# Performance work log

Measured on AMD Instinct MI355X. Metric: run time of the kernel, lower is better.

## Reference

```python
import jax, jax.numpy as jnp
import numpy as np

N = 10000      # nodes (= num_spatial_nodes)
E = 320000     # edges
IN = 4         # in_channels
HID = 256      # hidden_channels
H1, C1 = 4, 64 # conv1: heads, per-head out (hidden//heads)
EDIM = 1       # edge_feature_size
EPS = 1e-5


def _layernorm(x, g, b):
    mu = jnp.mean(x, axis=-1, keepdims=True)
    var = jnp.mean(jnp.square(x - mu), axis=-1, keepdims=True)
    return (x - mu) / jnp.sqrt(var + EPS) * g + b


def _gatv2(x, src, dst, ea, Wl, bl, Wr, br, We, att, bias, H, C, n):
    # PyG GATv2Conv: lin_l on source, lin_r on target, lin_edge on edge_attr
    xl = (x @ Wl + bl).reshape(n, H, C)
    xr = (x @ Wr + br).reshape(n, H, C)
    ee = (ea @ We).reshape(-1, H, C)
    m = jax.nn.leaky_relu(xl[src] + xr[dst] + ee, 0.2)   # [E', H, C]
    logit = jnp.einsum('ehc,hc->eh', m, att)             # [E', H]
    # segment softmax over incoming edges of each dst node
    mx = jax.ops.segment_max(logit, dst, num_segments=n)
    ex = jnp.exp(logit - mx[dst])
    den = jax.ops.segment_sum(ex, dst, num_segments=n)
    alpha = ex / den[dst]
    out = jax.ops.segment_sum(xl[src] * alpha[:, :, None], dst, num_segments=n)
    return out.reshape(n, H * C) + bias


def setup_inputs() -> dict:
    key = jax.random.key(0)
    ks = jax.random.split(key, 32)
    gl = lambda k, shape, fan: (jax.random.normal(k, shape, jnp.float32) / np.sqrt(fan)).astype(jnp.float32)
    inp = {}
    inp['x'] = jax.random.normal(ks[0], (N, IN), jnp.float32)
    inp['edge_index'] = jax.random.randint(ks[1], (2, E), 0, N, jnp.int32)
    inp['edge_attr'] = jax.random.normal(ks[2], (E, EDIM), jnp.float32)
    # conv1 (heads=4, out=64, concat -> 256)
    inp['Wl1'] = gl(ks[3], (IN, HID), IN);  inp['bl1'] = jnp.zeros((HID,), jnp.float32)
    inp['Wr1'] = gl(ks[4], (IN, HID), IN);  inp['br1'] = jnp.zeros((HID,), jnp.float32)
    inp['We1'] = gl(ks[5], (EDIM, HID), EDIM)
    inp['att1'] = gl(ks[6], (H1, C1), C1)
    inp['bias1'] = jnp.zeros((HID,), jnp.float32)
    inp['g1'] = jnp.ones((HID,), jnp.float32); inp['be1'] = jnp.zeros((HID,), jnp.float32)
    # conv2 (heads=1, out=256)
    inp['Wl2'] = gl(ks[7], (HID, HID), HID); inp['bl2'] = jnp.zeros((HID,), jnp.float32)
    inp['Wr2'] = gl(ks[8], (HID, HID), HID); inp['br2'] = jnp.zeros((HID,), jnp.float32)
    inp['We2'] = gl(ks[9], (EDIM, HID), EDIM)
    inp['att2'] = gl(ks[10], (1, HID), HID)
    inp['bias2'] = jnp.zeros((HID,), jnp.float32)
    inp['g2'] = jnp.ones((HID,), jnp.float32); inp['be2'] = jnp.zeros((HID,), jnp.float32)
    # policy head
    inp['Wp1'] = gl(ks[11], (HID, HID // 2), HID); inp['bp1'] = jnp.zeros((HID // 2,), jnp.float32)
    inp['Wp2'] = gl(ks[12], (HID // 2, IN), HID // 2); inp['bp2'] = jnp.zeros((IN,), jnp.float32)
    return inp


def reference(x, edge_index, edge_attr,
              Wl1, bl1, Wr1, br1, We1, att1, bias1, g1, be1,
              Wl2, bl2, Wr2, br2, We2, att2, bias2, g2, be2,
              Wp1, bp1, Wp2, bp2):
    src, dst = edge_index[0], edge_index[1]
    # add_self_loops with fill_value='mean': loop edge_attr = mean of incoming edge_attr
    deg = jax.ops.segment_sum(jnp.ones((E,), jnp.float32), dst, num_segments=N)
    loop_attr = jax.ops.segment_sum(edge_attr, dst, num_segments=N) / jnp.maximum(deg, 1.0)[:, None]
    ar = jnp.arange(N, dtype=src.dtype)
    src_a = jnp.concatenate([src, ar]); dst_a = jnp.concatenate([dst, ar])
    ea_a = jnp.concatenate([edge_attr, loop_attr], axis=0)
    h = _gatv2(x, src_a, dst_a, ea_a, Wl1, bl1, Wr1, br1, We1, att1, bias1, H1, C1, N)
    h = jax.nn.relu(_layernorm(h, g1, be1))
    h = _gatv2(h, src_a, dst_a, ea_a, Wl2, bl2, Wr2, br2, We2, att2, bias2, 1, HID, N)
    h = jax.nn.relu(_layernorm(h, g2, be2))
    logits = jax.nn.relu(h @ Wp1 + bp1) @ Wp2 + bp2   # [N, IN]
    return jax.nn.softmax(logits.reshape(1, -1), axis=1)
```

## Files before the change

kernel.cpp:

```cpp
#include <hip/hip_runtime.h>
#include <math.h>

#define N_NODES 10000
#define N_EDGES 320000
#define N_AUG   (N_EDGES + N_NODES)
#define CPK_CAP 330752
#define HID     256

typedef short short8 __attribute__((ext_vector_type(8)));
typedef float floatx16 __attribute__((ext_vector_type(16)));

static __device__ __forceinline__ unsigned bf16rne(float f) {
  unsigned u = __float_as_uint(f);
  return (u + 0x7FFFu + ((u >> 16) & 1u)) >> 16;
}

__global__ void __launch_bounds__(256) k_front(
    const int* __restrict__ dst, const float* __restrict__ ea,
    unsigned long long* __restrict__ pdeg, int* __restrict__ rank,
    const float* __restrict__ W1, const float* __restrict__ W2,
    const float* __restrict__ Wp1,
    unsigned short* __restrict__ Wt, unsigned short* __restrict__ Wp1t) {
  __shared__ float tile[32][33];
  int bi = blockIdx.x;
// ... 49 lines not shown
  for (int i = 0; i < 40; i++) {
    int n = base + i;
    if (n < N_NODES) s += (int)(pdeg[n] >> 32) + 1;
  }
  int v = s;
  #pragma unroll
  for (int d = 1; d < 64; d <<= 1) {
    int u = __shfl_up(v, d);
    if ((t & 63) >= d) v += u;
  }
  if ((t & 63) == 63) wsum[t >> 6] = v;
  __syncthreads();
  int wb = 0;
  for (int i = 0; i < (t >> 6); i++) wb += wsum[i];
  int run = wb + v - s;
  for (int i = 0; i < 40; i++) {
    int n = base + i;
    if (n < N_NODES) {
      offs[n] = run;
      unsigned long long pv = pdeg[n];
      int d = (int)(pv >> 32);
      run += d + 1;
      int lower = (int)(pv & 0xFFFFFFFFull);
      float asum = (float)(lower - d * 2097152) * (1.f / 262144.f);
      lattr[n] = asum / (float)max(d, 1);
    }
  }
  if (t == 255) offs[N_NODES] = wb + v;
}

__global__ void k_scatter(const int* __restrict__ src, const int* __restrict__ dst,
                          const float* __restrict__ ea, const float* __restrict__ lattr,
                          const int* __restrict__ offs, const int* __restrict__ rank,
                          int2* __restrict__ cpk) {
  int e = blockIdx.x * blockDim.x + threadIdx.x;
  if (e >= N_AUG) {
    if (e < CPK_CAP) cpk[e] = make_int2(0, 0);
    return;
  }
  int pos, s; float a;
  if (e < N_EDGES) {
    s = src[e];
    int d = dst[e];
    a = ea[e];
    pos = offs[d] + rank[e];
  } else {
    s = e - N_EDGES;
    a = lattr[s];
    pos = offs[s + 1] - 1;
  }
  cpk[pos] = make_int2(s, __float_as_int(a));
}

#define C1_EDGE(xs, av, l0, l1, l2, l3, p)                                              \
  {                                                                                     \
    l0 = fmaf(xs.x,wl0.x, fmaf(xs.y,wl1.x, fmaf(xs.z,wl2.x, fmaf(xs.w,wl3.x, blv.x)))); \
    l1 = fmaf(xs.x,wl0.y, fmaf(xs.y,wl1.y, fmaf(xs.z,wl2.y, fmaf(xs.w,wl3.y, blv.y)))); \
    l2 = fmaf(xs.x,wl0.z, fmaf(xs.y,wl1.z, fmaf(xs.z,wl2.z, fmaf(xs.w,wl3.z, blv.z)))); \
    l3 = fmaf(xs.x,wl0.w, fmaf(xs.y,wl1.w, fmaf(xs.z,wl2.w, fmaf(xs.w,wl3.w, blv.w)))); \
    float m0 = l0 + fmaf(av, we.x, r4.x); m0 = fmaxf(m0, 0.2f*m0);                      \
    float m1 = l1 + fmaf(av, we.y, r4.y); m1 = fmaxf(m1, 0.2f*m1);                      \
    float m2 = l2 + fmaf(av, we.z, r4.z); m2 = fmaxf(m2, 0.2f*m2);                      \
    float m3 = l3 + fmaf(av, we.w, r4.w); m3 = fmaxf(m3, 0.2f*m3);                      \
    p = m0*at.x + m1*at.y + m2*at.z + m3*at.w;                                          \
  }

#define C1_BODY8()                                                              \
  {                                                                             \
    float avA = __int_as_float(eA.y), avB = __int_as_float(eB.y);               \
    float avC = __int_as_float(eC.y), avD = __int_as_float(eD.y);               \
    float avE = __int_as_float(eE.y), avF = __int_as_float(eF.y);               \
    float avG = __int_as_float(eG.y), avH = __int_as_float(eH.y);               \
    float lA0,lA1,lA2,lA3,pA, lB0,lB1,lB2,lB3,pB;                               \
    float lC0,lC1,lC2,lC3,pC, lD0,lD1,lD2,lD3,pD;                               \
    float lE0,lE1,lE2,lE3,pE, lF0,lF1,lF2,lF3,pF;                               \
    float lG0,lG1,lG2,lG3,pG, lH0,lH1,lH2,lH3,pH;                               \
    C1_EDGE(xA, avA, lA0,lA1,lA2,lA3, pA);                                      \
    C1_EDGE(xB, avB, lB0,lB1,lB2,lB3, pB);                                      \
    C1_EDGE(xC, avC, lC0,lC1,lC2,lC3, pC);                                      \
    C1_EDGE(xD, avD, lD0,lD1,lD2,lD3, pD);                                      \
    C1_EDGE(xE, avE, lE0,lE1,lE2,lE3, pE);                                      \
    C1_EDGE(xF, avF, lF0,lF1,lF2,lF3, pF);                                      \
    C1_EDGE(xG, avG, lG0,lG1,lG2,lG3, pG);                                      \
    C1_EDGE(xH, avH, lH0,lH1,lH2,lH3, pH);                                      \
    float sAB = b1 ? pA : pB, kAB = b1 ? pB : pA;                               \
    float qAB = kAB + __shfl_xor(sAB, 1);                                       \
    float sCD = b1 ? pC : pD, kCD = b1 ? pD : pC;                               \
    float qCD = kCD + __shfl_xor(sCD, 1);                                       \
    float sEF = b1 ? pE : pF, kEF = b1 ? pF : pE;                               \
    float qEF = kEF + __shfl_xor(sEF, 1);                                       \
    float sGH = b1 ? pG : pH, kGH = b1 ? pH : pG;                               \
    float qGH = kGH + __shfl_xor(sGH, 1);                                       \
    float u0s = b2 ? qAB : qCD, u0k = b2 ? qCD : qAB;                           \
    float u0 = u0k + __shfl_xor(u0s, 2);                                        \
    float u1s = b2 ? qEF : qGH, u1k = b2 ? qGH : qEF;                           \
    float u1 = u1k + __shfl_xor(u1s, 2);                                        \
    float vvs = b4 ? u0 : u1, vvk = b4 ? u1 : u0;                               \
    float vv = vvk + __shfl_xor(vvs, 4);                                        \
    vv += __shfl_xor(vv, 8);                                                    \
    float exv = expf(vv);                                                       \
    float xAe = __shfl(exv, 0, 16), xBe = __shfl(exv, 1, 16);                   \
    float xCe = __shfl(exv, 2, 16), xDe = __shfl(exv, 3, 16);                   \
    float xEe = __shfl(exv, 4, 16), xFe = __shfl(exv, 5, 16);                   \
    float xGe = __shfl(exv, 6, 16), xHe = __shfl(exv, 7, 16);                   \
    D += ((xAe + xBe) + (xCe + xDe)) + ((xEe + xFe) + (xGe + xHe));             \
    a0 = fmaf(xDe, lD0, fmaf(xCe, lC0, fmaf(xBe, lB0, fmaf(xAe, lA0, a0))));    \
    a0 = fmaf(xHe, lH0, fmaf(xGe, lG0, fmaf(xFe, lF0, fmaf(xEe, lE0, a0))));    \
    a1 = fmaf(xDe, lD1, fmaf(xCe, lC1, fmaf(xBe, lB1, fmaf(xAe, lA1, a1))));    \
    a1 = fmaf(xHe, lH1, fmaf(xGe, lG1, fmaf(xFe, lF1, fmaf(xEe, lE1, a1))));    \
    a2 = fmaf(xDe, lD2, fmaf(xCe, lC2, fmaf(xBe, lB2, fmaf(xAe, lA2, a2))));    \
    a2 = fmaf(xHe, lH2, fmaf(xGe, lG2, fmaf(xFe, lF2, fmaf(xEe, lE2, a2))));    \
    a3 = fmaf(xDe, lD3, fmaf(xCe, lC3, fmaf(xBe, lB3, fmaf(xAe, lA3, a3))));    \
    a3 = fmaf(xHe, lH3, fmaf(xGe, lG3, fmaf(xFe, lF3, fmaf(xEe, lE3, a3))));    \
  }

__global__ void __launch_bounds__(256) k_conv1(
    const float* __restrict__ x,
    const float* __restrict__ Wl, const float* __restrict__ bl,
    const float* __restrict__ Wr, const float* __restrict__ br,
    const float* __restrict__ We, const float* __restrict__ att,
    const int* __restrict__ offs, const int2* __restrict__ cpk,
    const float* __restrict__ bias, const float* __restrict__ g,
    const float* __restrict__ be, uint2* __restrict__ h1b) {
  int t = threadIdx.x;
  int n = blockIdx.x * 4 + (t >> 6);
  int c = 4 * (t & 63);
  bool b1 = (t & 1) != 0, b2 = (t & 2) != 0, b4 = (t & 4) != 0;

  float4 wl0 = *(const float4*)&Wl[0*HID + c];
  float4 wl1 = *(const float4*)&Wl[1*HID + c];
  float4 wl2 = *(const float4*)&Wl[2*HID + c];
  float4 wl3 = *(const float4*)&Wl[3*HID + c];
  float4 blv = *(const float4*)&bl[c];
  float4 we  = *(const float4*)&We[c];
  float4 at  = *(const float4*)&att[c];

  float4 xn = *(const float4*)&x[n*4];
  float4 r4;
  {
    float4 wr0 = *(const float4*)&Wr[0*HID + c];
    float4 wr1 = *(const float4*)&Wr[1*HID + c];
    float4 wr2 = *(const float4*)&Wr[2*HID + c];
    float4 wr3 = *(const float4*)&Wr[3*HID + c];
    float4 brv = *(const float4*)&br[c];
    r4.x = fmaf(xn.x,wr0.x, fmaf(xn.y,wr1.x, fmaf(xn.z,wr2.x, fmaf(xn.w,wr3.x, brv.x))));
    r4.y = fmaf(xn.x,wr0.y, fmaf(xn.y,wr1.y, fmaf(xn.z,wr2.y, fmaf(xn.w,wr3.y, brv.y))));
    r4.z = fmaf(xn.x,wr0.z, fmaf(xn.y,wr1.z, fmaf(xn.z,wr2.z, fmaf(xn.w,wr3.z, brv.z))));
    r4.w = fmaf(xn.x,wr0.w, fmaf(xn.y,wr1.w, fmaf(xn.z,wr2.w, fmaf(xn.w,wr3.w, brv.w))));
  }

  int js = __builtin_amdgcn_readfirstlane(offs[n]);
  int je = __builtin_amdgcn_readfirstlane(offs[n+1]);

  float D = 0.f, a0 = 0.f, a1 = 0.f, a2 = 0.f, a3 = 0.f;

  int j = js;
  if (je - js >= 16) {
    int2 eA = cpk[j],   eB = cpk[j+1], eC = cpk[j+2], eD = cpk[j+3];
    int2 eE = cpk[j+4], eF = cpk[j+5], eG = cpk[j+6], eH = cpk[j+7];
    int2 fA = cpk[j+8],  fB = cpk[j+9],  fC = cpk[j+10], fD = cpk[j+11];
    int2 fE = cpk[j+12], fF = cpk[j+13], fG = cpk[j+14], fH = cpk[j+15];
    float4 xA = *(const float4*)&x[eA.x*4];
    float4 xB = *(const float4*)&x[eB.x*4];
    float4 xC = *(const float4*)&x[eC.x*4];
    float4 xD = *(const float4*)&x[eD.x*4];
    float4 xE = *(const float4*)&x[eE.x*4];
    float4 xF = *(const float4*)&x[eF.x*4];
    float4 xG = *(const float4*)&x[eG.x*4];
    float4 xH = *(const float4*)&x[eH.x*4];
    for (; j + 15 < je; j += 8) {
      float4 yA = *(const float4*)&x[fA.x*4];
      float4 yB = *(const float4*)&x[fB.x*4];
      float4 yC = *(const float4*)&x[fC.x*4];
      float4 yD = *(const float4*)&x[fD.x*4];
      float4 yE = *(const float4*)&x[fE.x*4];
      float4 yF = *(const float4*)&x[fF.x*4];
      float4 yG = *(const float4*)&x[fG.x*4];
      float4 yH = *(const float4*)&x[fH.x*4];
      int2 gA = cpk[j+16], gB = cpk[j+17], gC = cpk[j+18], gD = cpk[j+19];
      int2 gE = cpk[j+20], gF = cpk[j+21], gG = cpk[j+22], gH = cpk[j+23];
      C1_BODY8();
      eA = fA; eB = fB; eC = fC; eD = fD; eE = fE; eF = fF; eG = fG; eH = fH;
      fA = gA; fB = gB; fC = gC; fD = gD; fE = gE; fF = gF; fG = gG; fH = gH;
      xA = yA; xB = yB; xC = yC; xD = yD; xE = yE; xF = yF; xG = yG; xH = yH;
    }
    C1_BODY8();
    j += 8;
  }
  for (; j + 7 < je; j += 8) {
    int2 eA = cpk[j],   eB = cpk[j+1], eC = cpk[j+2], eD = cpk[j+3];
    int2 eE = cpk[j+4], eF = cpk[j+5], eG = cpk[j+6], eH = cpk[j+7];
    float4 xA = *(const float4*)&x[eA.x*4];
    float4 xB = *(const float4*)&x[eB.x*4];
    float4 xC = *(const float4*)&x[eC.x*4];
    float4 xD = *(const float4*)&x[eD.x*4];
    float4 xE = *(const float4*)&x[eE.x*4];
    float4 xF = *(const float4*)&x[eF.x*4];
    float4 xG = *(const float4*)&x[eG.x*4];
    float4 xH = *(const float4*)&x[eH.x*4];
    C1_BODY8();
  }
  for (; j < je; j++) {
    int2 eA = cpk[j];
    float4 xA = *(const float4*)&x[eA.x*4];
    float avA = __int_as_float(eA.y);
    float lA0,lA1,lA2,lA3,pA;
    C1_EDGE(xA, avA, lA0,lA1,lA2,lA3, pA);
    #pragma unroll
    for (int msk = 1; msk < 16; msk <<= 1) pA += __shfl_xor(pA, msk);
    float eAx = expf(pA);
    D += eAx;
    a0 = fmaf(eAx, lA0, a0);
    a1 = fmaf(eAx, lA1, a1);
    a2 = fmaf(eAx, lA2, a2);
    a3 = fmaf(eAx, lA3, a3);
  }

  float inv = 1.f / D;
  float4 b4v = *(const float4*)&bias[c];
  float o0 = fmaf(a0, inv, b4v.x);
  float o1 = fmaf(a1, inv, b4v.y);
  float o2 = fmaf(a2, inv, b4v.z);
  float o3 = fmaf(a3, inv, b4v.w);

  float s = o0 + o1 + o2 + o3;
  #pragma unroll
  for (int msk = 1; msk < 64; msk <<= 1) s += __shfl_xor(s, msk);
  float mu = s * (1.f / 256.f);
  float d0 = o0 - mu, d1 = o1 - mu, d2 = o2 - mu, d3 = o3 - mu;
  float sq = d0*d0 + d1*d1 + d2*d2 + d3*d3;
  #pragma unroll
  for (int msk = 1; msk < 64; msk <<= 1) sq += __shfl_xor(sq, msk);
  float rstd = rsqrtf(sq * (1.f / 256.f) + 1e-5f);
  float4 g4  = *(const float4*)&g[c];
  float4 be4 = *(const float4*)&be[c];
  float oy0 = fmaxf(fmaf(d0 * rstd, g4.x, be4.x), 0.f);
  float oy1 = fmaxf(fmaf(d1 * rstd, g4.y, be4.y), 0.f);
  float oy2 = fmaxf(fmaf(d2 * rstd, g4.z, be4.z), 0.f);
  float oy3 = fmaxf(fmaf(d3 * rstd, g4.w, be4.w), 0.f);
  uint2 pk;
  pk.x = bf16rne(oy0) | (bf16rne(oy1) << 16);
  pk.y = bf16rne(oy2) | (bf16rne(oy3) << 16);
  h1b[n*64 + (t & 63)] = pk;
}

#define C2_LOAD(q, xs)                                  \
  float4 xs;                                            \
  xs.x = __uint_as_float(q.x << 16);                    \
  xs.y = __uint_as_float(q.x & 0xFFFF0000u);            \
  xs.z = __uint_as_float(q.y << 16);                    \
  xs.w = __uint_as_float(q.y & 0xFFFF0000u);

#define C2_EDGE(xs, av, p)                                           \
  {                                                                  \
    float m0 = xs.x + fmaf(av, we.x, r4.x); m0 = fmaxf(m0, 0.2f*m0); \
    float m1 = xs.y + fmaf(av, we.y, r4.y); m1 = fmaxf(m1, 0.2f*m1); \
    float m2 = xs.z + fmaf(av, we.z, r4.z); m2 = fmaxf(m2, 0.2f*m2); \
    float m3 = xs.w + fmaf(av, we.w, r4.w); m3 = fmaxf(m3, 0.2f*m3); \
    p = m0*at.x + m1*at.y + m2*at.z + m3*at.w;                       \
  }

#define C2_PROC8()                                                              \
  {                                                                             \
    C2_LOAD(q0, xs0); C2_LOAD(q1, xs1); C2_LOAD(q2, xs2); C2_LOAD(q3, xs3);     \
    C2_LOAD(q4, xs4); C2_LOAD(q5, xs5); C2_LOAD(q6, xs6); C2_LOAD(q7, xs7);     \
    float av0 = __int_as_float(e0.y), av1 = __int_as_float(e1.y);               \
    float av2 = __int_as_float(e2.y), av3 = __int_as_float(e3.y);               \
    float av4 = __int_as_float(e4.y), av5 = __int_as_float(e5.y);               \
    float av6 = __int_as_float(e6.y), av7 = __int_as_float(e7.y);               \
    float p0,p1,p2,p3,p4,p5,p6,p7;                                              \
    C2_EDGE(xs0, av0, p0); C2_EDGE(xs1, av1, p1);                               \
    C2_EDGE(xs2, av2, p2); C2_EDGE(xs3, av3, p3);                               \
    C2_EDGE(xs4, av4, p4); C2_EDGE(xs5, av5, p5);                               \
    C2_EDGE(xs6, av6, p6); C2_EDGE(xs7, av7, p7);                               \
    float sAB = b1 ? p0 : p1, kAB = b1 ? p1 : p0;                               \
    float qAB = kAB + __shfl_xor(sAB, 1);                                       \
    float sCD = b1 ? p2 : p3, kCD = b1 ? p3 : p2;                               \
    float qCD = kCD + __shfl_xor(sCD, 1);                                       \
    float sEF = b1 ? p4 : p5, kEF = b1 ? p5 : p4;                               \
    float qEF = kEF + __shfl_xor(sEF, 1);                                       \
    float sGH = b1 ? p6 : p7, kGH = b1 ? p7 : p6;                               \
    float qGH = kGH + __shfl_xor(sGH, 1);                                       \
    float u0s = b2 ? qAB : qCD, u0k = b2 ? qCD : qAB;                           \
    float u0 = u0k + __shfl_xor(u0s, 2);                                        \
    float u1s = b2 ? qEF : qGH, u1k = b2 ? qGH : qEF;                           \
    float u1 = u1k + __shfl_xor(u1s, 2);                                        \
    float vvs = b4 ? u0 : u1, vvk = b4 ? u1 : u0;                               \
    float vv = vvk + __shfl_xor(vvs, 4);                                        \
    vv += __shfl_xor(vv, 8);                                                    \
    vv += __shfl_xor(vv, 16);                                                   \
    vv += __shfl_xor(vv, 32);                                                   \
    float exv = expf(vv);                                                       \
    float x0 = __shfl(exv, 0), x1 = __shfl(exv, 1);                             \
    float x2 = __shfl(exv, 2), x3 = __shfl(exv, 3);                             \
    float x4 = __shfl(exv, 4), x5 = __shfl(exv, 5);                             \
    float x6 = __shfl(exv, 6), x7 = __shfl(exv, 7);                             \
    D += ((x0 + x1) + (x2 + x3)) + ((x4 + x5) + (x6 + x7));                     \
    a0 = fmaf(x3, xs3.x, fmaf(x2, xs2.x, fmaf(x1, xs1.x, fmaf(x0, xs0.x, a0))));\
    a0 = fmaf(x7, xs7.x, fmaf(x6, xs6.x, fmaf(x5, xs5.x, fmaf(x4, xs4.x, a0))));\
    a1 = fmaf(x3, xs3.y, fmaf(x2, xs2.y, fmaf(x1, xs1.y, fmaf(x0, xs0.y, a1))));\
    a1 = fmaf(x7, xs7.y, fmaf(x6, xs6.y, fmaf(x5, xs5.y, fmaf(x4, xs4.y, a1))));\
    a2 = fmaf(x3, xs3.z, fmaf(x2, xs2.z, fmaf(x1, xs1.z, fmaf(x0, xs0.z, a2))));\
    a2 = fmaf(x7, xs7.z, fmaf(x6, xs6.z, fmaf(x5, xs5.z, fmaf(x4, xs4.z, a2))));\
    a3 = fmaf(x3, xs3.w, fmaf(x2, xs2.w, fmaf(x1, xs1.w, fmaf(x0, xs0.w, a3))));\
    a3 = fmaf(x7, xs7.w, fmaf(x6, xs6.w, fmaf(x5, xs5.w, fmaf(x4, xs4.w, a3))));\
  }

__global__ void __launch_bounds__(256) k_conv2(
    const uint2* __restrict__ xlb, const uint2* __restrict__ xrb,
    const int* __restrict__ offs, const int2* __restrict__ cpk,
    const float* __restrict__ We, const float* __restrict__ att,
    const float* __restrict__ bias, const float* __restrict__ g,
    const float* __restrict__ be, uint2* __restrict__ h2b) {
  int t = threadIdx.x;
  int n = blockIdx.x * 4 + (t >> 6);
  int lane = t & 63;
  int c = 4 * lane;
  bool b1 = (t & 1) != 0, b2 = (t & 2) != 0, b4 = (t & 4) != 0;
  uint2 rq = xrb[n*64 + lane];
  C2_LOAD(rq, r4);
  float4 we = *(const float4*)&We[c];
  float4 at = *(const float4*)&att[c];
  int js = __builtin_amdgcn_readfirstlane(offs[n]);
  int je = __builtin_amdgcn_readfirstlane(offs[n+1]);

  float D = 0.f, a0 = 0.f, a1 = 0.f, a2 = 0.f, a3 = 0.f;

  int j = js;
  if (je - js >= 16) {
    int2 e0 = cpk[j],   e1 = cpk[j+1], e2 = cpk[j+2], e3 = cpk[j+3];
    int2 e4 = cpk[j+4], e5 = cpk[j+5], e6 = cpk[j+6], e7 = cpk[j+7];
    int2 f0 = cpk[j+8],  f1 = cpk[j+9],  f2 = cpk[j+10], f3 = cpk[j+11];
    int2 f4 = cpk[j+12], f5 = cpk[j+13], f6 = cpk[j+14], f7 = cpk[j+15];
    uint2 q0 = xlb[e0.x*64 + lane];
    uint2 q1 = xlb[e1.x*64 + lane];
    uint2 q2 = xlb[e2.x*64 + lane];
    uint2 q3 = xlb[e3.x*64 + lane];
    uint2 q4 = xlb[e4.x*64 + lane];
    uint2 q5 = xlb[e5.x*64 + lane];
    uint2 q6 = xlb[e6.x*64 + lane];
    uint2 q7 = xlb[e7.x*64 + lane];
    for (; j + 15 < je; j += 8) {
      uint2 r0 = xlb[f0.x*64 + lane];
      uint2 r1 = xlb[f1.x*64 + lane];
      uint2 r2 = xlb[f2.x*64 + lane];
      uint2 r3 = xlb[f3.x*64 + lane];
      uint2 r4_ = xlb[f4.x*64 + lane];
      uint2 r5 = xlb[f5.x*64 + lane];
      uint2 r6 = xlb[f6.x*64 + lane];
      uint2 r7 = xlb[f7.x*64 + lane];
      int2 g0 = cpk[j+16], g1 = cpk[j+17], g2 = cpk[j+18], g3 = cpk[j+19];
      int2 g4 = cpk[j+20], g5 = cpk[j+21], g6 = cpk[j+22], g7 = cpk[j+23];
      C2_PROC8();
      e0 = f0; e1 = f1; e2 = f2; e3 = f3; e4 = f4; e5 = f5; e6 = f6; e7 = f7;
      f0 = g0; f1 = g1; f2 = g2; f3 = g3; f4 = g4; f5 = g5; f6 = g6; f7 = g7;
      q0 = r0; q1 = r1; q2 = r2; q3 = r3; q4 = r4_; q5 = r5; q6 = r6; q7 = r7;
    }
    C2_PROC8();
    j += 8;
  }
  for (; j + 7 < je; j += 8) {
    int2 e0 = cpk[j],   e1 = cpk[j+1], e2 = cpk[j+2], e3 = cpk[j+3];
    int2 e4 = cpk[j+4], e5 = cpk[j+5], e6 = cpk[j+6], e7 = cpk[j+7];
    uint2 q0 = xlb[e0.x*64 + lane];
    uint2 q1 = xlb[e1.x*64 + lane];
    uint2 q2 = xlb[e2.x*64 + lane];
    uint2 q3 = xlb[e3.x*64 + lane];
    uint2 q4 = xlb[e4.x*64 + lane];
    uint2 q5 = xlb[e5.x*64 + lane];
    uint2 q6 = xlb[e6.x*64 + lane];
    uint2 q7 = xlb[e7.x*64 + lane];
    C2_PROC8();
  }
  for (; j < je; j++) {
    int2 e0 = cpk[j];
    float av0 = __int_as_float(e0.y);
    uint2 q0 = xlb[e0.x*64 + lane];
    C2_LOAD(q0, xs0);
    float p0;
    C2_EDGE(xs0, av0, p0);
    #pragma unroll
    for (int msk = 1; msk < 64; msk <<= 1) p0 += __shfl_xor(p0, msk);
    float x0 = expf(p0);
    D += x0;
    a0 = fmaf(x0, xs0.x, a0);
    a1 = fmaf(x0, xs0.y, a1);
    a2 = fmaf(x0, xs0.z, a2);
    a3 = fmaf(x0, xs0.w, a3);
  }

  float inv = 1.f / D;
  float4 b4v = *(const float4*)&bias[c];
  float o0 = fmaf(a0, inv, b4v.x);
  float o1 = fmaf(a1, inv, b4v.y);
  float o2 = fmaf(a2, inv, b4v.z);
  float o3 = fmaf(a3, inv, b4v.w);

  float s = o0 + o1 + o2 + o3;
  #pragma unroll
  for (int msk = 1; msk < 64; msk <<= 1) s += __shfl_xor(s, msk);
  float mu = s * (1.f / 256.f);
  float d0 = o0 - mu, d1 = o1 - mu, d2 = o2 - mu, d3 = o3 - mu;
  float sq = d0*d0 + d1*d1 + d2*d2 + d3*d3;
  #pragma unroll
  for (int msk = 1; msk < 64; msk <<= 1) sq += __shfl_xor(sq, msk);
  float rstd = rsqrtf(sq * (1.f / 256.f) + 1e-5f);
  float4 g4  = *(const float4*)&g[c];
  float4 be4 = *(const float4*)&be[c];
  float oy0 = fmaxf(fmaf(d0 * rstd, g4.x, be4.x), 0.f);
  float oy1 = fmaxf(fmaf(d1 * rstd, g4.y, be4.y), 0.f);
  float oy2 = fmaxf(fmaf(d2 * rstd, g4.z, be4.z), 0.f);
  float oy3 = fmaxf(fmaf(d3 * rstd, g4.w, be4.w), 0.f);
  uint2 pk;
  pk.x = bf16rne(oy0) | (bf16rne(oy1) << 16);
  pk.y = bf16rne(oy2) | (bf16rne(oy3) << 16);
  h2b[n*64 + lane] = pk;
}

__global__ void __launch_bounds__(256) k_gemm_dual(
    const unsigned short* __restrict__ h1b, const unsigned short* __restrict__ Wt,
    const float* __restrict__ b1, const float* __restrict__ b2,
    unsigned short* __restrict__ O1b, unsigned short* __restrict__ O2b) {
  __shared__ unsigned short A_lds[64][72];
  __shared__ unsigned short W_lds[128][72];
  int t = threadIdx.x;
  int r0 = blockIdx.x * 64;
  int nb0 = blockIdx.y * 128;
  int l = t & 63;
  int wave = t >> 6;
  int wr = wave >> 1, wc = wave & 1;

  floatx16 acc[2] = {{0}, {0}};

  int sar = t >> 2, sak = (t & 3) * 16;
  int arow = min(r0 + sar, N_NODES - 1);
  int swn = t >> 1, swk = (t & 1) * 32;
  const unsigned short* Wrow = &Wt[(nb0 + swn) * 256];

  for (int kb = 0; kb < 256; kb += 64) {
    uint4 av0 = *(const uint4*)&h1b[arow*256 + kb + sak];
    uint4 av1 = *(const uint4*)&h1b[arow*256 + kb + sak + 8];
    uint4 wv0 = *(const uint4*)&Wrow[kb + swk];
    uint4 wv1 = *(const uint4*)&Wrow[kb + swk + 8];
    uint4 wv2 = *(const uint4*)&Wrow[kb + swk + 16];
    uint4 wv3 = *(const uint4*)&Wrow[kb + swk + 24];
    __syncthreads();
    *(uint4*)&A_lds[sar][sak]     = av0;
    *(uint4*)&A_lds[sar][sak + 8] = av1;
    *(uint4*)&W_lds[swn][swk]      = wv0;
    *(uint4*)&W_lds[swn][swk +  8] = wv1;
    *(uint4*)&W_lds[swn][swk + 16] = wv2;
    *(uint4*)&W_lds[swn][swk + 24] = wv3;
    __syncthreads();
    #pragma unroll
    for (int ks = 0; ks < 64; ks += 16) {
      short8 af  = *(const short8*)&A_lds[wr*32 + (l & 31)][ks + 8*(l >> 5)];
      short8 bf0 = *(const short8*)&W_lds[wc*64      + (l & 31)][ks + 8*(l >> 5)];
      short8 bf1 = *(const short8*)&W_lds[wc*64 + 32 + (l & 31)][ks + 8*(l >> 5)];
      acc[0] = __builtin_amdgcn_mfma_f32_32x32x16_bf16(af, bf0, acc[0], 0, 0, 0);
      acc[1] = __builtin_amdgcn_mfma_f32_32x32x16_bf16(af, bf1, acc[1], 0, 0, 0);
    }
  }

  bool isO1 = (nb0 < 256);
  #pragma unroll
  for (int tile = 0; tile < 2; tile++) {
    int col = nb0 + wc*64 + tile*32 + (l & 31);
    float bias = isO1 ? b1[col] : b2[col - 256];
    #pragma unroll
// ... 102 lines not shown
                              void* d_out, int out_size, void* d_ws, size_t ws_size,
                              hipStream_t stream) {
  const float* x    = (const float*)d_in[0];
  const int*   ei   = (const int*)  d_in[1];
  const float* ea   = (const float*)d_in[2];
  const float* Wl1  = (const float*)d_in[3];
  const float* bl1  = (const float*)d_in[4];
  const float* Wr1  = (const float*)d_in[5];
  const float* br1  = (const float*)d_in[6];
  const float* We1  = (const float*)d_in[7];
  const float* att1 = (const float*)d_in[8];
  const float* bias1= (const float*)d_in[9];
  const float* g1   = (const float*)d_in[10];
  const float* be1  = (const float*)d_in[11];
  const float* Wl2  = (const float*)d_in[12];
  const float* bl2  = (const float*)d_in[13];
  const float* Wr2  = (const float*)d_in[14];
  const float* br2  = (const float*)d_in[15];
  const float* We2  = (const float*)d_in[16];
  const float* att2 = (const float*)d_in[17];
  const float* bias2= (const float*)d_in[18];
  const float* g2   = (const float*)d_in[19];
  const float* be2  = (const float*)d_in[20];
  const float* Wp1  = (const float*)d_in[21];
  const float* bp1  = (const float*)d_in[22];
  const float* Wp2  = (const float*)d_in[23];
  const float* bp2  = (const float*)d_in[24];
  float* out = (float*)d_out;

  const int* srcp = ei;
  const int* dstp = ei + N_EDGES;

  unsigned long long* pdeg = (unsigned long long*)d_ws;
  float* tot   = (float*)(pdeg + 10240);
  int*   offs  = (int*)(tot + 16);
  float* lattr = (float*)(offs + 10240);
  int*   rank  = (int*)(lattr + 10240);
  int2*  cpk   = (int2*)(rank + 320192);
  unsigned short* h1b   = (unsigned short*)(cpk + CPK_CAP);
  unsigned short* h2b   = h1b;
  unsigned short* xl2bf = h1b + 2560000;
  unsigned short* xr2b  = xl2bf + 2560000;
  float* elg   = (float*)(xr2b + 2560000);
  unsigned short* Wt   = (unsigned short*)(elg + 40960);
  unsigned short* Wp1t = Wt + 512*256;

  hipMemsetAsync(pdeg, 0, 10240 * 8 + 64, stream);

  k_front  <<<1250 + 192, 256, 0, stream>>>(dstp, ea, pdeg, rank,
                                            Wl2, Wr2, Wp1, Wt, Wp1t);
  k_scan   <<<1, 256, 0, stream>>>(pdeg, offs, lattr);
  k_scatter<<<(CPK_CAP + 255)/256, 256, 0, stream>>>(srcp, dstp, ea, lattr, offs,
                                                     rank, cpk);
  k_conv1  <<<N_NODES/4, 256, 0, stream>>>(x, Wl1, bl1, Wr1, br1, We1, att1,
                                           offs, cpk, bias1, g1, be1, (uint2*)h1b);
  k_gemm_dual<<<dim3(157, 4), 256, 0, stream>>>(h1b, Wt, bl2, br2, xl2bf, xr2b);
  k_conv2  <<<N_NODES/4, 256, 0, stream>>>((const uint2*)xl2bf, (const uint2*)xr2b,
                                           offs, cpk, We2, att2, bias2, g2, be2,
                                           (uint2*)h2b);
  k_policy <<<157, 256, 0, stream>>>(h2b, Wp1t, bp1, Wp2, bp2, elg, tot);
  k_sm_final<<<40, 1024, 0, stream>>>(elg, tot, out);
}
```

Before: 252.5 us.

## Split each node across two waves with two channels per lane in GAT convs

Both GATv2 aggregation kernels now give each node its own 128-thread block. Each of the two waves handles 128 channels at 2 channels per lane, where before one wave covered all 256 channels at 4 per lane. The aim is to double the number of waves working on the edge gathers, giving more memory-level parallelism and fewer registers per thread. In exchange, conv2 needs a cross-wave exchange of attention logits through shared memory with a __syncthreads for every 8-edge group, and LayerNorm statistics are combined through LDS. Each loaded xl element is also narrower (4 bytes instead of 8).

Result: slower. 260.1 us (+3.0%).

```diff
diff --git a/kernel.cpp b/kernel.cpp
--- a/kernel.cpp
+++ b/kernel.cpp
@@ -125,17 +125,13 @@
   cpk[pos] = make_int2(s, __float_as_int(a));
 }
 
-#define C1_EDGE(xs, av, l0, l1, l2, l3, p)                                              \
-  {                                                                                     \
+#define C1_EDGE2(xs, av, l0, l1, p)                                             \
+  {                                                                             \
     l0 = fmaf(xs.x,wl0.x, fmaf(xs.y,wl1.x, fmaf(xs.z,wl2.x, fmaf(xs.w,wl3.x, blv.x)))); \
     l1 = fmaf(xs.x,wl0.y, fmaf(xs.y,wl1.y, fmaf(xs.z,wl2.y, fmaf(xs.w,wl3.y, blv.y)))); \
-    l2 = fmaf(xs.x,wl0.z, fmaf(xs.y,wl1.z, fmaf(xs.z,wl2.z, fmaf(xs.w,wl3.z, blv.z)))); \
-    l3 = fmaf(xs.x,wl0.w, fmaf(xs.y,wl1.w, fmaf(xs.z,wl2.w, fmaf(xs.w,wl3.w, blv.w)))); \
-    float m0 = l0 + fmaf(av, we.x, r4.x); m0 = fmaxf(m0, 0.2f*m0);                      \
-    float m1 = l1 + fmaf(av, we.y, r4.y); m1 = fmaxf(m1, 0.2f*m1);                      \
-    float m2 = l2 + fmaf(av, we.z, r4.z); m2 = fmaxf(m2, 0.2f*m2);                      \
-    float m3 = l3 + fmaf(av, we.w, r4.w); m3 = fmaxf(m3, 0.2f*m3);                      \
-    p = m0*at.x + m1*at.y + m2*at.z + m3*at.w;                                          \
+    float m0 = l0 + fmaf(av, we2.x, r40); m0 = fmaxf(m0, 0.2f*m0);              \
+    float m1 = l1 + fmaf(av, we2.y, r41); m1 = fmaxf(m1, 0.2f*m1);              \
+    p = m0*at2.x + m1*at2.y;                                                    \
   }
 
 #define C1_BODY8()                                                              \
@@ -144,18 +140,16 @@
     float avC = __int_as_float(eC.y), avD = __int_as_float(eD.y);               \
     float avE = __int_as_float(eE.y), avF = __int_as_float(eF.y);               \
     float avG = __int_as_float(eG.y), avH = __int_as_float(eH.y);               \
-    float lA0,lA1,lA2,lA3,pA, lB0,lB1,lB2,lB3,pB;                               \
-    float lC0,lC1,lC2,lC3,pC, lD0,lD1,lD2,lD3,pD;                               \
-    float lE0,lE1,lE2,lE3,pE, lF0,lF1,lF2,lF3,pF;                               \
-    float lG0,lG1,lG2,lG3,pG, lH0,lH1,lH2,lH3,pH;                               \
-    C1_EDGE(xA, avA, lA0,lA1,lA2,lA3, pA);                                      \
-    C1_EDGE(xB, avB, lB0,lB1,lB2,lB3, pB);                                      \
-    C1_EDGE(xC, avC, lC0,lC1,lC2,lC3, pC);                                      \
-    C1_EDGE(xD, avD, lD0,lD1,lD2,lD3, pD);                                      \
-    C1_EDGE(xE, avE, lE0,lE1,lE2,lE3, pE);                                      \
-    C1_EDGE(xF, avF, lF0,lF1,lF2,lF3, pF);                                      \
-    C1_EDGE(xG, avG, lG0,lG1,lG2,lG3, pG);                                      \
-    C1_EDGE(xH, avH, lH0,lH1,lH2,lH3, pH);                                      \
+    float lA0,lA1,pA, lB0,lB1,pB, lC0,lC1,pC, lD0,lD1,pD;                       \
+    float lE0,lE1,pE, lF0,lF1,pF, lG0,lG1,pG, lH0,lH1,pH;                       \
+    C1_EDGE2(xA, avA, lA0,lA1, pA);                                             \
+    C1_EDGE2(xB, avB, lB0,lB1, pB);                                             \
+    C1_EDGE2(xC, avC, lC0,lC1, pC);                                             \
+    C1_EDGE2(xD, avD, lD0,lD1, pD);                                             \
+    C1_EDGE2(xE, avE, lE0,lE1, pE);                                             \
+    C1_EDGE2(xF, avF, lF0,lF1, pF);                                             \
+    C1_EDGE2(xG, avG, lG0,lG1, pG);                                             \
+    C1_EDGE2(xH, avH, lH0,lH1, pH);                                             \
     float sAB = b1 ? pA : pB, kAB = b1 ? pB : pA;                               \
     float qAB = kAB + __shfl_xor(sAB, 1);                                       \
     float sCD = b1 ? pC : pD, kCD = b1 ? pD : pC;                               \
@@ -171,61 +165,58 @@
     float vvs = b4 ? u0 : u1, vvk = b4 ? u1 : u0;                               \
     float vv = vvk + __shfl_xor(vvs, 4);                                        \
     vv += __shfl_xor(vv, 8);                                                    \
+    vv += __shfl_xor(vv, 16);                                                   \
     float exv = expf(vv);                                                       \
-    float xAe = __shfl(exv, 0, 16), xBe = __shfl(exv, 1, 16);                   \
-    float xCe = __shfl(exv, 2, 16), xDe = __shfl(exv, 3, 16);                   \
-    float xEe = __shfl(exv, 4, 16), xFe = __shfl(exv, 5, 16);                   \
-    float xGe = __shfl(exv, 6, 16), xHe = __shfl(exv, 7, 16);                   \
+    float xAe = __shfl(exv, 0, 32), xBe = __shfl(exv, 1, 32);                   \
+    float xCe = __shfl(exv, 2, 32), xDe = __shfl(exv, 3, 32);                   \
+    float xEe = __shfl(exv, 4, 32), xFe = __shfl(exv, 5, 32);                   \
+    float xGe = __shfl(exv, 6, 32), xHe = __shfl(exv, 7, 32);                   \
     D += ((xAe + xBe) + (xCe + xDe)) + ((xEe + xFe) + (xGe + xHe));             \
     a0 = fmaf(xDe, lD0, fmaf(xCe, lC0, fmaf(xBe, lB0, fmaf(xAe, lA0, a0))));    \
     a0 = fmaf(xHe, lH0, fmaf(xGe, lG0, fmaf(xFe, lF0, fmaf(xEe, lE0, a0))));    \
     a1 = fmaf(xDe, lD1, fmaf(xCe, lC1, fmaf(xBe, lB1, fmaf(xAe, lA1, a1))));    \
     a1 = fmaf(xHe, lH1, fmaf(xGe, lG1, fmaf(xFe, lF1, fmaf(xEe, lE1, a1))));    \
-    a2 = fmaf(xDe, lD2, fmaf(xCe, lC2, fmaf(xBe, lB2, fmaf(xAe, lA2, a2))));    \
-    a2 = fmaf(xHe, lH2, fmaf(xGe, lG2, fmaf(xFe, lF2, fmaf(xEe, lE2, a2))));    \
-    a3 = fmaf(xDe, lD3, fmaf(xCe, lC3, fmaf(xBe, lB3, fmaf(xAe, lA3, a3))));    \
-    a3 = fmaf(xHe, lH3, fmaf(xGe, lG3, fmaf(xFe, lF3, fmaf(xEe, lE3, a3))));    \
-  }
-
-__global__ void __launch_bounds__(256) k_conv1(
+  }
+
+__global__ void __launch_bounds__(128) k_conv1(
     const float* __restrict__ x,
     const float* __restrict__ Wl, const float* __restrict__ bl,
     const float* __restrict__ Wr, const float* __restrict__ br,
     const float* __restrict__ We, const float* __restrict__ att,
     const int* __restrict__ offs, const int2* __restrict__ cpk,
     const float* __restrict__ bias, const float* __restrict__ g,
-    const float* __restrict__ be, uint2* __restrict__ h1b) {
+    const float* __restrict__ be, unsigned* __restrict__ h1u) {
+  __shared__ float lnA[2], lnB[2];
   int t = threadIdx.x;
-  int n = blockIdx.x * 4 + (t >> 6);
-  int c = 4 * (t & 63);
-  bool b1 = (t & 1) != 0, b2 = (t & 2) != 0, b4 = (t & 4) != 0;
-
-  float4 wl0 = *(const float4*)&Wl[0*HID + c];
-  float4 wl1 = *(const float4*)&Wl[1*HID + c];
-  float4 wl2 = *(const float4*)&Wl[2*HID + c];
-  float4 wl3 = *(const float4*)&Wl[3*HID + c];
-  float4 blv = *(const float4*)&bl[c];
-  float4 we  = *(const float4*)&We[c];
-  float4 at  = *(const float4*)&att[c];
+  int w = t >> 6, l = t & 63;
+  int n = blockIdx.x;
+  int c = w*128 + 2*l;
+  bool b1 = (l & 1) != 0, b2 = (l & 2) != 0, b4 = (l & 4) != 0;
+
+  float2 wl0 = *(const float2*)&Wl[0*HID + c];
+  float2 wl1 = *(const float2*)&Wl[1*HID + c];
+  float2 wl2 = *(const float2*)&Wl[2*HID + c];
+  float2 wl3 = *(const float2*)&Wl[3*HID + c];
+  float2 blv = *(const float2*)&bl[c];
+  float2 we2 = *(const float2*)&We[c];
+  float2 at2 = *(const float2*)&att[c];
 
   float4 xn = *(const float4*)&x[n*4];
-  float4 r4;
+  float r40, r41;
   {
-    float4 wr0 = *(const float4*)&Wr[0*HID + c];
-    float4 wr1 = *(const float4*)&Wr[1*HID + c];
-    float4 wr2 = *(const float4*)&Wr[2*HID + c];
-    float4 wr3 = *(const float4*)&Wr[3*HID + c];
-    float4 brv = *(const float4*)&br[c];
-    r4.x = fmaf(xn.x,wr0.x, fmaf(xn.y,wr1.x, fmaf(xn.z,wr2.x, fmaf(xn.w,wr3.x, brv.x))));
-    r4.y = fmaf(xn.x,wr0.y, fmaf(xn.y,wr1.y, fmaf(xn.z,wr2.y, fmaf(xn.w,wr3.y, brv.y))));
-    r4.z = fmaf(xn.x,wr0.z, fmaf(xn.y,wr1.z, fmaf(xn.z,wr2.z, fmaf(xn.w,wr3.z, brv.z))));
-    r4.w = fmaf(xn.x,wr0.w, fmaf(xn.y,wr1.w, fmaf(xn.z,wr2.w, fmaf(xn.w,wr3.w, brv.w))));
+    float2 wr0 = *(const float2*)&Wr[0*HID + c];
+    float2 wr1 = *(const float2*)&Wr[1*HID + c];
+    float2 wr2 = *(const float2*)&Wr[2*HID + c];
+    float2 wr3 = *(const float2*)&Wr[3*HID + c];
+    float2 brv = *(const float2*)&br[c];
+    r40 = fmaf(xn.x,wr0.x, fmaf(xn.y,wr1.x, fmaf(xn.z,wr2.x, fmaf(xn.w,wr3.x, brv.x))));
+    r41 = fmaf(xn.x,wr0.y, fmaf(xn.y,wr1.y, fmaf(xn.z,wr2.y, fmaf(xn.w,wr3.y, brv.y))));
   }
 
   int js = __builtin_amdgcn_readfirstlane(offs[n]);
   int je = __builtin_amdgcn_readfirstlane(offs[n+1]);
 
-  float D = 0.f, a0 = 0.f, a1 = 0.f, a2 = 0.f, a3 = 0.f;
+  float D = 0.f, a0 = 0.f, a1 = 0.f;
 
   int j = js;
   if (je - js >= 16) {
@@ -277,75 +268,67 @@
     int2 eA = cpk[j];
     float4 xA = *(const float4*)&x[eA.x*4];
     float avA = __int_as_float(eA.y);
-    float lA0,lA1,lA2,lA3,pA;
-    C1_EDGE(xA, avA, lA0,lA1,lA2,lA3, pA);
-    #pragma unroll
-    for (int msk = 1; msk < 16; msk <<= 1) pA += __shfl_xor(pA, msk);
+    float lA0,lA1,pA;
+    C1_EDGE2(xA, avA, lA0,lA1, pA);
+    #pragma unroll
+    for (int msk = 1; msk < 32; msk <<= 1) pA += __shfl_xor(pA, msk);
     float eAx = expf(pA);
     D += eAx;
     a0 = fmaf(eAx, lA0, a0);
     a1 = fmaf(eAx, lA1, a1);
-    a2 = fmaf(eAx, lA2, a2);
-    a3 = fmaf(eAx, lA3, a3);
   }
 
   float inv = 1.f / D;
-  float4 b4v = *(const float4*)&bias[c];
-  float o0 = fmaf(a0, inv, b4v.x);
-  float o1 = fmaf(a1, inv, b4v.y);
-  float o2 = fmaf(a2, inv, b4v.z);
-  float o3 = fmaf(a3, inv, b4v.w);
-
-  float s = o0 + o1 + o2 + o3;
+  float2 b2v = *(const float2*)&bias[c];
+  float o0 = fmaf(a0, inv, b2v.x);
+  float o1 = fmaf(a1, inv, b2v.y);
+
+  float s = o0 + o1;
   #pragma unroll
   for (int msk = 1; msk < 64; msk <<= 1) s += __shfl_xor(s, msk);
-  float mu = s * (1.f / 256.f);
-  float d0 = o0 - mu, d1 = o1 - mu, d2 = o2 - mu, d3 = o3 - mu;
-  float sq = d0*d0 + d1*d1 + d2*d2 + d3*d3;
+  if (l == 0) lnA[w] = s;
+  __syncthreads();
+  float mu = (lnA[0] + lnA[1]) * (1.f / 256.f);
+  float d0 = o0 - mu, d1 = o1 - mu;
+  float sq = d0*d0 + d1*d1;
   #pragma unroll
   for (int msk = 1; msk < 64; msk <<= 1) sq += __shfl_xor(sq, msk);
-  float rstd = rsqrtf(sq * (1.f / 256.f) + 1e-5f);
-  float4 g4  = *(const float4*)&g[c];
-  float4 be4 = *(const float4*)&be[c];
-  float oy0 = fmaxf(fmaf(d0 * rstd, g4.x, be4.x), 0.f);
-  float oy1 = fmaxf(fmaf(d1 * rstd, g4.y, be4.y), 0.f);
-  float oy2 = fmaxf(fmaf(d2 * rstd, g4.z, be4.z), 0.f);
-  float oy3 = fmaxf(fmaf(d3 * rstd, g4.w, be4.w), 0.f);
-  uint2 pk;
-  pk.x = bf16rne(oy0) | (bf16rne(oy1) << 16);
-  pk.y = bf16rne(oy2) | (bf16rne(oy3) << 16);
-  h1b[n*64 + (t & 63)] = pk;
-}
-
-#define C2_LOAD(q, xs)                                  \
-  float4 xs;                                            \
-  xs.x = __uint_as_float(q.x << 16);                    \
-  xs.y = __uint_as_float(q.x & 0xFFFF0000u);            \
-  xs.z = __uint_as_float(q.y << 16);                    \
-  xs.w = __uint_as_float(q.y & 0xFFFF0000u);
-
-#define C2_EDGE(xs, av, p)                                           \
+  if (l == 0) lnB[w] = sq;
+  __syncthreads();
+  float rstd = rsqrtf((lnB[0] + lnB[1]) * (1.f / 256.f) + 1e-5f);
+  float2 g2v  = *(const float2*)&g[c];
+  float2 be2v = *(const float2*)&be[c];
+  float oy0 = fmaxf(fmaf(d0 * rstd, g2v.x, be2v.x), 0.f);
+  float oy1 = fmaxf(fmaf(d1 * rstd, g2v.y, be2v.y), 0.f);
+  h1u[n*128 + w*64 + l] = bf16rne(oy0) | (bf16rne(oy1) << 16);
+}
+
+#define C2_EDGE2(x0v, x1v, av, p)                                    \
   {                                                                  \
-    float m0 = xs.x + fmaf(av, we.x, r4.x); m0 = fmaxf(m0, 0.2f*m0); \
-    float m1 = xs.y + fmaf(av, we.y, r4.y); m1 = fmaxf(m1, 0.2f*m1); \
-    float m2 = xs.z + fmaf(av, we.z, r4.z); m2 = fmaxf(m2, 0.2f*m2); \
-    float m3 = xs.w + fmaf(av, we.w, r4.w); m3 = fmaxf(m3, 0.2f*m3); \
-    p = m0*at.x + m1*at.y + m2*at.z + m3*at.w;                       \
+    float m0 = x0v + fmaf(av, we2.x, r40); m0 = fmaxf(m0, 0.2f*m0);  \
+    float m1 = x1v + fmaf(av, we2.y, r41); m1 = fmaxf(m1, 0.2f*m1);  \
+    p = m0*at2.x + m1*at2.y;                                         \
   }
 
 #define C2_PROC8()                                                              \
   {                                                                             \
-    C2_LOAD(q0, xs0); C2_LOAD(q1, xs1); C2_LOAD(q2, xs2); C2_LOAD(q3, xs3);     \
-    C2_LOAD(q4, xs4); C2_LOAD(q5, xs5); C2_LOAD(q6, xs6); C2_LOAD(q7, xs7);     \
+    float xs00 = __uint_as_float(q0 << 16), xs01 = __uint_as_float(q0 & 0xFFFF0000u); \
+    float xs10 = __uint_as_float(q1 << 16), xs11 = __uint_as_float(q1 & 0xFFFF0000u); \
+    float xs20 = __uint_as_float(q2 << 16), xs21 = __uint_as_float(q2 & 0xFFFF0000u); \
+    float xs30 = __uint_as_float(q3 << 16), xs31 = __uint_as_float(q3 & 0xFFFF0000u); \
+    float xs40 = __uint_as_float(q4 << 16), xs41 = __uint_as_float(q4 & 0xFFFF0000u); \
+    float xs50 = __uint_as_float(q5 << 16), xs51 = __uint_as_float(q5 & 0xFFFF0000u); \
+    float xs60 = __uint_as_float(q6 << 16), xs61 = __uint_as_float(q6 & 0xFFFF0000u); \
+    float xs70 = __uint_as_float(q7 << 16), xs71 = __uint_as_float(q7 & 0xFFFF0000u); \
     float av0 = __int_as_float(e0.y), av1 = __int_as_float(e1.y);               \
     float av2 = __int_as_float(e2.y), av3 = __int_as_float(e3.y);               \
     float av4 = __int_as_float(e4.y), av5 = __int_as_float(e5.y);               \
     float av6 = __int_as_float(e6.y), av7 = __int_as_float(e7.y);               \
     float p0,p1,p2,p3,p4,p5,p6,p7;                                              \
-    C2_EDGE(xs0, av0, p0); C2_EDGE(xs1, av1, p1);                               \
-    C2_EDGE(xs2, av2, p2); C2_EDGE(xs3, av3, p3);                               \
-    C2_EDGE(xs4, av4, p4); C2_EDGE(xs5, av5, p5);                               \
-    C2_EDGE(xs6, av6, p6); C2_EDGE(xs7, av7, p7);                               \
+    C2_EDGE2(xs00, xs01, av0, p0); C2_EDGE2(xs10, xs11, av1, p1);               \
+    C2_EDGE2(xs20, xs21, av2, p2); C2_EDGE2(xs30, xs31, av3, p3);               \
+    C2_EDGE2(xs40, xs41, av4, p4); C2_EDGE2(xs50, xs51, av5, p5);               \
+    C2_EDGE2(xs60, xs61, av6, p6); C2_EDGE2(xs70, xs71, av7, p7);               \
     float sAB = b1 ? p0 : p1, kAB = b1 ? p1 : p0;                               \
     float qAB = kAB + __shfl_xor(sAB, 1);                                       \
     float sCD = b1 ? p2 : p3, kCD = b1 ? p3 : p2;                               \
@@ -363,41 +346,47 @@
     vv += __shfl_xor(vv, 8);                                                    \
     vv += __shfl_xor(vv, 16);                                                   \
     vv += __shfl_xor(vv, 32);                                                   \
-    float exv = expf(vv);                                                       \
+    if (l < 8) xch[par][w][l] = vv;                                             \
+    __syncthreads();                                                            \
+    float vvt = vv + xch[par][1 - w][l & 7];                                    \
+    par ^= 1;                                                                   \
+    float exv = expf(vvt);                                                      \
     float x0 = __shfl(exv, 0), x1 = __shfl(exv, 1);                             \
     float x2 = __shfl(exv, 2), x3 = __shfl(exv, 3);                             \
     float x4 = __shfl(exv, 4), x5 = __shfl(exv, 5);                             \
     float x6 = __shfl(exv, 6), x7 = __shfl(exv, 7);                             \
     D += ((x0 + x1) + (x2 + x3)) + ((x4 + x5) + (x6 + x7));                     \
-    a0 = fmaf(x3, xs3.x, fmaf(x2, xs2.x, fmaf(x1, xs1.x, fmaf(x0, xs0.x, a0))));\
-    a0 = fmaf(x7, xs7.x, fmaf(x6, xs6.x, fmaf(x5, xs5.x, fmaf(x4, xs4.x, a0))));\
-    a1 = fmaf(x3, xs3.y, fmaf(x2, xs2.y, fmaf(x1, xs1.y, fmaf(x0, xs0.y, a1))));\
-    a1 = fmaf(x7, xs7.y, fmaf(x6, xs6.y, fmaf(x5, xs5.y, fmaf(x4, xs4.y, a1))));\
-    a2 = fmaf(x3, xs3.z, fmaf(x2, xs2.z, fmaf(x1, xs1.z, fmaf(x0, xs0.z, a2))));\
-    a2 = fmaf(x7, xs7.z, fmaf(x6, xs6.z, fmaf(x5, xs5.z, fmaf(x4, xs4.z, a2))));\
-    a3 = fmaf(x3, xs3.w, fmaf(x2, xs2.w, fmaf(x1, xs1.w, fmaf(x0, xs0.w, a3))));\
-    a3 = fmaf(x7, xs7.w, fmaf(x6, xs6.w, fmaf(x5, xs5.w, fmaf(x4, xs4.w, a3))));\
-  }
-
-__global__ void __launch_bounds__(256) k_conv2(
-    const uint2* __restrict__ xlb, const uint2* __restrict__ xrb,
+    a0 = fmaf(x3, xs30, fmaf(x2, xs20, fmaf(x1, xs10, fmaf(x0, xs00, a0))));    \
+    a0 = fmaf(x7, xs70, fmaf(x6, xs60, fmaf(x5, xs50, fmaf(x4, xs40, a0))));    \
+    a1 = fmaf(x3, xs31, fmaf(x2, xs21, fmaf(x1, xs11, fmaf(x0, xs01, a1))));    \
+    a1 = fmaf(x7, xs71, fmaf(x6, xs61, fmaf(x5, xs51, fmaf(x4, xs41, a1))));    \
+  }
+
+__global__ void __launch_bounds__(128) k_conv2(
+    const unsigned* __restrict__ xlu, const unsigned* __restrict__ xru,
     const int* __restrict__ offs, const int2* __restrict__ cpk,
     const float* __restrict__ We, const float* __restrict__ att,
     const float* __restrict__ bias, const float* __restrict__ g,
-    const float* __restrict__ be, uint2* __restrict__ h2b) {
+    const float* __restrict__ be, unsigned* __restrict__ h2u) {
+  __shared__ float xch[2][2][8];
+  __shared__ float lnA[2], lnB[2];
   int t = threadIdx.x;
-  int n = blockIdx.x * 4 + (t >> 6);
-  int lane = t & 63;
-  int c = 4 * lane;
-  bool b1 = (t & 1) != 0, b2 = (t & 2) != 0, b4 = (t & 4) != 0;
-  uint2 rq = xrb[n*64 + lane];
-  C2_LOAD(rq, r4);
-  float4 we = *(const float4*)&We[c];
-  float4 at = *(const float4*)&att[c];
+  int w = t >> 6, l = t & 63;
+  int n = blockIdx.x;
+  int c = w*128 + 2*l;
+  bool b1 = (l & 1) != 0, b2 = (l & 2) != 0, b4 = (l & 4) != 0;
+  int par = 0;
+
+  unsigned rq = xru[n*128 + w*64 + l];
+  float r40 = __uint_as_float(rq << 16);
+  float r41 = __uint_as_float(rq & 0xFFFF0000u);
+  float2 we2 = *(const float2*)&We[c];
+  float2 at2 = *(const float2*)&att[c];
   int js = __builtin_amdgcn_readfirstlane(offs[n]);
   int je = __builtin_amdgcn_readfirstlane(offs[n+1]);
 
-  float D = 0.f, a0 = 0.f, a1 = 0.f, a2 = 0.f, a3 = 0.f;
+  float D = 0.f, a0 = 0.f, a1 = 0.f;
+  int rowoff = w*64 + l;
 
   int j = js;
   if (je - js >= 16) {
@@ -405,23 +394,23 @@
     int2 e4 = cpk[j+4], e5 = cpk[j+5], e6 = cpk[j+6], e7 = cpk[j+7];
     int2 f0 = cpk[j+8],  f1 = cpk[j+9],  f2 = cpk[j+10], f3 = cpk[j+11];
     int2 f4 = cpk[j+12], f5 = cpk[j+13], f6 = cpk[j+14], f7 = cpk[j+15];
-    uint2 q0 = xlb[e0.x*64 + lane];
-    uint2 q1 = xlb[e1.x*64 + lane];
-    uint2 q2 = xlb[e2.x*64 + lane];
-    uint2 q3 = xlb[e3.x*64 + lane];
-    uint2 q4 = xlb[e4.x*64 + lane];
-    uint2 q5 = xlb[e5.x*64 + lane];
-    uint2 q6 = xlb[e6.x*64 + lane];
-    uint2 q7 = xlb[e7.x*64 + lane];
+    unsigned q0 = xlu[e0.x*128 + rowoff];
+    unsigned q1 = xlu[e1.x*128 + rowoff];
+    unsigned q2 = xlu[e2.x*128 + rowoff];
+    unsigned q3 = xlu[e3.x*128 + rowoff];
+    unsigned q4 = xlu[e4.x*128 + rowoff];
+    unsigned q5 = xlu[e5.x*128 + rowoff];
+    unsigned q6 = xlu[e6.x*128 + rowoff];
+    unsigned q7 = xlu[e7.x*128 + rowoff];
     for (; j + 15 < je; j += 8) {
-      uint2 r0 = xlb[f0.x*64 + lane];
-      uint2 r1 = xlb[f1.x*64 + lane];
-      uint2 r2 = xlb[f2.x*64 + lane];
-      uint2 r3 = xlb[f3.x*64 + lane];
-      uint2 r4_ = xlb[f4.x*64 + lane];
-      uint2 r5 = xlb[f5.x*64 + lane];
-      uint2 r6 = xlb[f6.x*64 + lane];
-      uint2 r7 = xlb[f7.x*64 + lane];
+      unsigned r0 = xlu[f0.x*128 + rowoff];
+      unsigned r1 = xlu[f1.x*128 + rowoff];
+      unsigned r2 = xlu[f2.x*128 + rowoff];
+      unsigned r3 = xlu[f3.x*128 + rowoff];
+      unsigned r4_ = xlu[f4.x*128 + rowoff];
+      unsigned r5 = xlu[f5.x*128 + rowoff];
+      unsigned r6 = xlu[f6.x*128 + rowoff];
+      unsigned r7 = xlu[f7.x*128 + rowoff];
       int2 g0 = cpk[j+16], g1 = cpk[j+17], g2 = cpk[j+18], g3 = cpk[j+19];
       int2 g4 = cpk[j+20], g5 = cpk[j+21], g6 = cpk[j+22], g7 = cpk[j+23];
       C2_PROC8();
@@ -435,59 +424,59 @@
   for (; j + 7 < je; j += 8) {
     int2 e0 = cpk[j],   e1 = cpk[j+1], e2 = cpk[j+2], e3 = cpk[j+3];
     int2 e4 = cpk[j+4], e5 = cpk[j+5], e6 = cpk[j+6], e7 = cpk[j+7];
-    uint2 q0 = xlb[e0.x*64 + lane];
-    uint2 q1 = xlb[e1.x*64 + lane];
-    uint2 q2 = xlb[e2.x*64 + lane];
-    uint2 q3 = xlb[e3.x*64 + lane];
-    uint2 q4 = xlb[e4.x*64 + lane];
-    uint2 q5 = xlb[e5.x*64 + lane];
-    uint2 q6 = xlb[e6.x*64 + lane];
-    uint2 q7 = xlb[e7.x*64 + lane];
+    unsigned q0 = xlu[e0.x*128 + rowoff];
+    unsigned q1 = xlu[e1.x*128 + rowoff];
+    unsigned q2 = xlu[e2.x*128 + rowoff];
+    unsigned q3 = xlu[e3.x*128 + rowoff];
+    unsigned q4 = xlu[e4.x*128 + rowoff];
+    unsigned q5 = xlu[e5.x*128 + rowoff];
+    unsigned q6 = xlu[e6.x*128 + rowoff];
+    unsigned q7 = xlu[e7.x*128 + rowoff];
     C2_PROC8();
   }
   for (; j < je; j++) {
     int2 e0 = cpk[j];
     float av0 = __int_as_float(e0.y);
-    uint2 q0 = xlb[e0.x*64 + lane];
-    C2_LOAD(q0, xs0);
+    unsigned q0 = xlu[e0.x*128 + rowoff];
+    float xs00 = __uint_as_float(q0 << 16);
+    float xs01 = __uint_as_float(q0 & 0xFFFF0000u);
     float p0;
-    C2_EDGE(xs0, av0, p0);
+    C2_EDGE2(xs00, xs01, av0, p0);
     #pragma unroll
     for (int msk = 1; msk < 64; msk <<= 1) p0 += __shfl_xor(p0, msk);
-    float x0 = expf(p0);
+    if (l == 0) xch[par][w][0] = p0;
+    __syncthreads();
+    float pt = p0 + xch[par][1 - w][0];
+    par ^= 1;
+    float x0 = expf(pt);
     D += x0;
-    a0 = fmaf(x0, xs0.x, a0);
-    a1 = fmaf(x0, xs0.y, a1);
-    a2 = fmaf(x0, xs0.z, a2);
-    a3 = fmaf(x0, xs0.w, a3);
+    a0 = fmaf(x0, xs00, a0);
+    a1 = fmaf(x0, xs01, a1);
   }
 
   float inv = 1.f / D;
-  float4 b4v = *(const float4*)&bias[c];
-  float o0 = fmaf(a0, inv, b4v.x);
-  float o1 = fmaf(a1, inv, b4v.y);
-  float o2 = fmaf(a2, inv, b4v.z);
-  float o3 = fmaf(a3, inv, b4v.w);
-
-  float s = o0 + o1 + o2 + o3;
+  float2 b2v = *(const float2*)&bias[c];
+  float o0 = fmaf(a0, inv, b2v.x);
+  float o1 = fmaf(a1, inv, b2v.y);
+
+  float s = o0 + o1;
   #pragma unroll
   for (int msk = 1; msk < 64; msk <<= 1) s += __shfl_xor(s, msk);
-  float mu = s * (1.f / 256.f);
-  float d0 = o0 - mu, d1 = o1 - mu, d2 = o2 - mu, d3 = o3 - mu;
-  float sq = d0*d0 + d1*d1 + d2*d2 + d3*d3;
+  if (l == 0) lnA[w] = s;
+  __syncthreads();
+  float mu = (lnA[0] + lnA[1]) * (1.f / 256.f);
+  float d0 = o0 - mu, d1 = o1 - mu;
+  float sq = d0*d0 + d1*d1;
   #pragma unroll
   for (int msk = 1; msk < 64; msk <<= 1) sq += __shfl_xor(sq, msk);
-  float rstd = rsqrtf(sq * (1.f / 256.f) + 1e-5f);
-  float4 g4  = *(const float4*)&g[c];
-  float4 be4 = *(const float4*)&be[c];
-  float oy0 = fmaxf(fmaf(d0 * rstd, g4.x, be4.x), 0.f);
-  float oy1 = fmaxf(fmaf(d1 * rstd, g4.y, be4.y), 0.f);
-  float oy2 = fmaxf(fmaf(d2 * rstd, g4.z, be4.z), 0.f);
-  float oy3 = fmaxf(fmaf(d3 * rstd, g4.w, be4.w), 0.f);
-  uint2 pk;
-  pk.x = bf16rne(oy0) | (bf16rne(oy1) << 16);
-  pk.y = bf16rne(oy2) | (bf16rne(oy3) << 16);
-  h2b[n*64 + lane] = pk;
+  if (l == 0) lnB[w] = sq;
+  __syncthreads();
+  float rstd = rsqrtf((lnB[0] + lnB[1]) * (1.f / 256.f) + 1e-5f);
+  float2 g2v  = *(const float2*)&g[c];
+  float2 be2v = *(const float2*)&be[c];
+  float oy0 = fmaxf(fmaf(d0 * rstd, g2v.x, be2v.x), 0.f);
+  float oy1 = fmaxf(fmaf(d1 * rstd, g2v.y, be2v.y), 0.f);
+  h2u[n*128 + w*64 + l] = bf16rne(oy0) | (bf16rne(oy1) << 16);
 }
 
 __global__ void __launch_bounds__(256) k_gemm_dual(
@@ -696,12 +685,12 @@
   k_scan   <<<1, 256, 0, stream>>>(pdeg, offs, lattr);
   k_scatter<<<(CPK_CAP + 255)/256, 256, 0, stream>>>(srcp, dstp, ea, lattr, offs,
                                                      rank, cpk);
-  k_conv1  <<<N_NODES/4, 256, 0, stream>>>(x, Wl1, bl1, Wr1, br1, We1, att1,
-                                           offs, cpk, bias1, g1, be1, (uint2*)h1b);
+  k_conv1  <<<N_NODES, 128, 0, stream>>>(x, Wl1, bl1, Wr1, br1, We1, att1,
+                                         offs, cpk, bias1, g1, be1, (unsigned*)h1b);
   k_gemm_dual<<<dim3(157, 4), 256, 0, stream>>>(h1b, Wt, bl2, br2, xl2bf, xr2b);
-  k_conv2  <<<N_NODES/4, 256, 0, stream>>>((const uint2*)xl2bf, (const uint2*)xr2b,
-                                           offs, cpk, We2, att2, bias2, g2, be2,
-                                           (uint2*)h2b);
+  k_conv2  <<<N_NODES, 128, 0, stream>>>((const unsigned*)xl2bf, (const unsigned*)xr2b,
+                                         offs, cpk, We2, att2, bias2, g2, be2,
+                                         (unsigned*)h2b);
   k_policy <<<157, 256, 0, stream>>>(h2b, Wp1t, bp1, Wp2, bp2, elg, tot);
   k_sm_final<<<40, 1024, 0, stream>>>(elg, tot, out);
 }
```
